# Kernel optimization log

Measured on AMD Instinct MI355X. Metric: run time of the kernel, lower is better.

The kernel has to match this reference:

```python
import jax, jax.numpy as jnp
import numpy as np

NUM_HEADS = 8

def setup_inputs() -> dict:
    key = jax.random.key(0)
    ks = jax.random.split(key, 8)
    B, T, J, N, C = 4, 16, 17, 17, 256
    x = jax.random.normal(ks[0], (B, T, J, N, C), dtype=jnp.float32)
    A_s = jax.random.uniform(ks[1], (J, J), dtype=jnp.float32)
    A_v = jax.random.uniform(ks[2], (N, N), dtype=jnp.float32)
    W_qkv = jax.random.normal(ks[3], (C, 5 * C), dtype=jnp.float32) * (C ** -0.5)
    W_proj = jax.random.normal(ks[4], (3 * C, C), dtype=jnp.float32) * ((3 * C) ** -0.5)
    b_proj = jnp.zeros((C,), dtype=jnp.float32)
    # M ~ xavier_uniform(gain=1.414) over shape (1, J, N, C)
    bound = 1.414 * np.sqrt(6.0 / (N + C))
    M = jax.random.uniform(ks[5], (1, J, N, C), dtype=jnp.float32, minval=-bound, maxval=bound)
    adj_s = jnp.full((J, J), 1e-6, dtype=jnp.float32)  # torch stores (1,1,J,J); broadcast-identical
    adj_v = jnp.full((N, N), 1e-6, dtype=jnp.float32)
    return {"x": x, "A_s": A_s, "A_v": A_v, "W_qkv": W_qkv, "W_proj": W_proj,
            "b_proj": b_proj, "M": M, "adj_s": adj_s, "adj_v": adj_v}


def reference(x, A_s, A_v, W_qkv, W_proj, b_proj, M, adj_s, adj_v):
    B, T, J, N, C = x.shape
    h = NUM_HEADS
    hc = C // h
    scale = hc ** -0.5
    bt = B * T
    xr = x.reshape(bt, J, N, C)
    # qkv Linear (no bias) then view(..., C, 5): channel-interleaved split
    qkv = (xr @ W_qkv).reshape(bt, J, N, C, 5)
    q, k, vs, vv, vsv = (qkv[..., i] * M for i in range(5))
    def heads(t):
        return t.reshape(bt, J, N, h, hc)
    q, k, vs, vv, vsv = map(heads, (q, k, vs, vv, vsv))
    # spatial attention over joints j (per node n), temporal/variate attention over n (per j)
    att_s_o = jnp.einsum('bjnhc,bknhc->bhnjk', q, k) * scale   # (bt,h,N,J,J)
    att_v_o = jnp.einsum('bjnhc,bjmhc->bhjnm', q, k) * scale   # (bt,h,J,N,N)
    att_s = jax.nn.softmax(att_s_o, axis=-1)
    att_v = jax.nn.softmax(att_v_o, axis=-1)
    # outer-product combine, algebraically separated:
    # x_vsv[b,j,n,:] = sum_{k,m} att_s[b,h,n,j,k] * att_v[b,h,j,n,m] * vsv[b,k,m,h,:]
    r = jnp.einsum('bhjnm,bkmhc->bhjnkc', att_v, vsv)           # (bt,h,J,N,J,hc)
    x_vsv = jnp.einsum('bhnjk,bhjnkc->bjnhc', att_s, r).reshape(bt, J, N, C)
    # adjacency-biased attentions (symmetrized learned bias + fixed adjacency)
    adjs = A_s + adj_s
    adjs = (adjs.T + adjs) * 0.5
    adjv = A_v + adj_v
    adjv = (adjv.T + adjv) * 0.5
    att_s2 = jax.nn.softmax(att_s_o + adjs, axis=-1)
    att_v2 = jax.nn.softmax(att_v_o + adjv, axis=-1)
    x_vs = jnp.einsum('bhnjk,bknhc->bjnhc', att_s2, vs).reshape(bt, J, N, C)
    x_vv = jnp.einsum('bhjnm,bjmhc->bjnhc', att_v2, vv).reshape(bt, J, N, C)
    out = jnp.concatenate([x_vsv, x_vs, x_vv], axis=-1) @ W_proj + b_proj
    return out.reshape(B, T, J, N, C)
```

## Files before the change

kernel.cpp:

```cpp
#include <hip/hip_runtime.h>
#include <math.h>

#define ROWS 18496
#define SCALE 0.17677669529663687f

typedef unsigned short ushort_t;
typedef __attribute__((ext_vector_type(8))) short short8;
typedef __attribute__((ext_vector_type(4))) float f32x4;

__device__ __forceinline__ void fma4(float4& d, float s, const float4& v) {
    d.x = fmaf(s, v.x, d.x); d.y = fmaf(s, v.y, d.y);
    d.z = fmaf(s, v.z, d.z); d.w = fmaf(s, v.w, d.w);
}
__device__ __forceinline__ float dot4(const float4& a, const float4& b) {
    return a.x*b.x + a.y*b.y + a.z*b.z + a.w*b.w;
}

__device__ __forceinline__ ushort_t f2bf(float x) {
    union { float f; unsigned u; } v; v.f = x;
    unsigned r = v.u + 0x7fffu + ((v.u >> 16) & 1u);
    return (ushort_t)(r >> 16);
}
__device__ __forceinline__ float bf2f(ushort_t b) {
    union { unsigned u; float f; } v; v.u = ((unsigned)b) << 16; return v.f;
}

__device__ __forceinline__ void gl_lds16(const void* g, void* l) {
    __builtin_amdgcn_global_load_lds(
        (const __attribute__((address_space(1))) void*)g,
        (__attribute__((address_space(3))) void*)l, 16, 0, 0);
}

__device__ __forceinline__ void store_hilo(ushort_t* yhi, ushort_t* ylo,
                                           size_t off, const float4& a)
{
    ushort4 h, l;
    h.x = f2bf(a.x); l.x = f2bf(a.x - bf2f(h.x));
    h.y = f2bf(a.y); l.y = f2bf(a.y - bf2f(h.y));
    h.z = f2bf(a.z); l.z = f2bf(a.z - bf2f(h.z));
    h.w = f2bf(a.w); l.w = f2bf(a.w - bf2f(h.w));
    *(ushort4*)&yhi[off] = h;
    *(ushort4*)&ylo[off] = l;
}

__global__ __launch_bounds__(256) void k_cvt_xw(
    const float4* __restrict__ x, ushort4* __restrict__ xhi, ushort4* __restrict__ xlo,
    const float* __restrict__ W, ushort_t* __restrict__ bh, ushort_t* __restrict__ bl)
{
    if (blockIdx.x < 4624) {
        int i = blockIdx.x * 256 + threadIdx.x;
        float4 v = x[i];
        ushort4 h, l;
        h.x = f2bf(v.x); l.x = f2bf(v.x - bf2f(h.x));
        h.y = f2bf(v.y); l.y = f2bf(v.y - bf2f(h.y));
        h.z = f2bf(v.z); l.z = f2bf(v.z - bf2f(h.z));
        h.w = f2bf(v.w); l.w = f2bf(v.w - bf2f(h.w));
        xhi[i] = h; xlo[i] = l;
    } else {
        int o = blockIdx.x - 4624;
        int kk = threadIdx.x;
        int col = (o & 255) * 5 + (o >> 8);
        float v = W[(size_t)kk * 1280 + col];
        ushort_t hh = f2bf(v);
        bh[(size_t)o * 256 + kk] = hh;
        bl[(size_t)o * 256 + kk] = f2bf(v - bf2f(hh));
    }
}

__global__ __launch_bounds__(256) void k_cvt_wp(
    const float* __restrict__ W, ushort_t* __restrict__ bh, ushort_t* __restrict__ bl)
{
    int n = blockIdx.x;
    for (int k = threadIdx.x; k < 768; k += 256) {
        float v = W[(size_t)k * 256 + n];
        ushort_t h = f2bf(v);
        bh[(size_t)n * 768 + k] = h;
        bl[(size_t)n * 768 + k] = f2bf(v - bf2f(h));
    }
}

template<int BM, int BN, int K, int MODE>
__global__ __launch_bounds__(256) void k_gemm(
    const ushort_t* __restrict__ Ahi, const ushort_t* __restrict__ Alo,
    const ushort_t* __restrict__ Bhi, const ushort_t* __restrict__ Blo,
    const float* __restrict__ aux,
    float* __restrict__ out)
{
    constexpr int MT = BM / 32;
    constexpr int NT = BN / 32;
    __shared__ __attribute__((aligned(16))) ushort_t sAh[BM * 32];
    __shared__ __attribute__((aligned(16))) ushort_t sAl[BM * 32];
    __shared__ __attribute__((aligned(16))) ushort_t sBh[BN * 32];
    __shared__ __attribute__((aligned(16))) ushort_t sBl[BN * 32];

    const int t = threadIdx.x;
    const int lane = t & 63;
    const int ln = lane & 15, quad = lane >> 4;
    const int wave = t >> 6;
    const int wm = wave >> 1, wn = wave & 1;
    const int m0 = blockIdx.y * BM, n0 = blockIdx.x * BN;

    f32x4 acc[MT][NT];
#pragma unroll
    for (int i = 0; i < MT; ++i)
#pragma unroll
        for (int j = 0; j < NT; ++j) acc[i][j] = (f32x4){0.f, 0.f, 0.f, 0.f};

    for (int kb = 0; kb < K; kb += 32) {
        __syncthreads();
#pragma unroll
        for (int s = t; s < BM * 4; s += 256) {
            int row = s >> 2, kc = s & 3;
            int gr = m0 + row; if (gr > ROWS - 1) gr = ROWS - 1;
            size_t gb = ((size_t)gr * K + kb) * 2 + kc * 16;
            int lb = (s & ~63) * 16;
            gl_lds16((const char*)Ahi + gb, (char*)sAh + lb);
            gl_lds16((const char*)Alo + gb, (char*)sAl + lb);
        }
#pragma unroll
        for (int s = t; s < BN * 4; s += 256) {
            int row = s >> 2, kc = s & 3;
            size_t gb = ((size_t)(n0 + row) * K + kb) * 2 + kc * 16;
            int lb = (s & ~63) * 16;
            gl_lds16((const char*)Bhi + gb, (char*)sBh + lb);
            gl_lds16((const char*)Blo + gb, (char*)sBl + lb);
        }
        __syncthreads();

        short8 ah[MT], al[MT], bh[NT], bl[NT];
#pragma unroll
        for (int i = 0; i < MT; ++i) {
            int off = (wm * (BM / 2) + i * 16 + ln) * 32 + quad * 8;
            ah[i] = *(const short8*)&sAh[off];
            al[i] = *(const short8*)&sAl[off];
        }
#pragma unroll
        for (int j = 0; j < NT; ++j) {
            int off = (wn * (BN / 2) + j * 16 + ln) * 32 + quad * 8;
            bh[j] = *(const short8*)&sBh[off];
            bl[j] = *(const short8*)&sBl[off];
        }
#pragma unroll
        for (int i = 0; i < MT; ++i)
#pragma unroll
            for (int j = 0; j < NT; ++j) {
                acc[i][j] = __builtin_amdgcn_mfma_f32_16x16x32_bf16(ah[i], bh[j], acc[i][j], 0, 0, 0);
                acc[i][j] = __builtin_amdgcn_mfma_f32_16x16x32_bf16(ah[i], bl[j], acc[i][j], 0, 0, 0);
                acc[i][j] = __builtin_amdgcn_mfma_f32_16x16x32_bf16(al[i], bh[j], acc[i][j], 0, 0, 0);
            }
    }

#pragma unroll
    for (int i = 0; i < MT; ++i) {
#pragma unroll
        for (int r = 0; r < 4; ++r) {
            int gm = m0 + wm * (BM / 2) + i * 16 + quad * 4 + r;
            if (gm >= ROWS) continue;
            if (MODE == 0) {
                int jn = gm % 289;
                const float* Mrow = &aux[(size_t)jn * 256];
#pragma unroll
                for (int j = 0; j < NT; ++j) {
                    int gn = n0 + wn * (BN / 2) + j * 16 + ln;
                    out[(size_t)gm * 1280 + gn] = acc[i][j][r] * Mrow[gn & 255];
                }
            } else {
#pragma unroll
                for (int j = 0; j < NT; ++j) {
                    int gn = n0 + wn * (BN / 2) + j * 16 + ln;
                    out[(size_t)gm * 256 + gn] = acc[i][j][r] + aux[gn];
                }
            }
        }
    }
}

__global__ __launch_bounds__(512, 2) void k_att(
    const float* __restrict__ qkv5,
    const float* __restrict__ A_s, const float* __restrict__ A_v,
    const float* __restrict__ adjS, const float* __restrict__ adjV,
    ushort_t* __restrict__ yhi, ushort_t* __restrict__ ylo)
{
    __shared__ __attribute__((aligned(16))) float sm[16184];
    float* aS  = sm;
    float* aV  = sm + 4913;
    float* ebS = sm + 9826;
    float* ebV = sm + 10115;
    float* buf = sm + 10404;

    const int t  = threadIdx.x;
    const int bh = blockIdx.x;
    const int b  = bh >> 3, h = bh & 7;
    const size_t rowbase = (size_t)b * 289;

    for (int idx = t; idx < 578; idx += 512) {
        int f = idx / 289, rem = idx % 289;
        int jj = rem / 17, kk = rem % 17;
        float bias;
        if (f == 0)
            bias = 0.5f * ((A_s[jj*17+kk] + adjS[jj*17+kk]) + (A_s[kk*17+jj] + adjS[kk*17+jj]));
        else
            bias = 0.5f * ((A_v[jj*17+kk] + adjV[jj*17+kk]) + (A_v[kk*17+jj] + adjV[kk*17+jj]));
        (f ? ebV : ebS)[rem] = expf(bias);
    }

    for (int ch = 0; ch < 2; ++ch) {
        __syncthreads();
        for (int idx = t; idx < 1156; idx += 512) {
            int p = idx >> 2, c = idx & 3;
            *(float4*)&buf[p * 20 + c * 4] =
                *(const float4*)&qkv5[(rowbase + p) * 1280 + 256 + h * 32 + ch * 16 + c * 4];
        }
        __syncthreads();
        for (int u = t; u < 578; u += 512) {
            const bool isS = (u < 289);
            const int p = isS ? u : u - 289;
            const float* qp = &qkv5[(rowbase + p) * 1280 + h * 32 + ch * 16];
            float4 q0 = *(const float4*)&qp[0];
            float4 q1 = *(const float4*)&qp[4];
            float4 q2 = *(const float4*)&qp[8];
            float4 q3 = *(const float4*)&qp[12];
            const int a = p / 17, bb = p % 17;
            float tmp[17];
            if (isS) {
#pragma unroll
                for (int kk = 0; kk < 17; ++kk) {
                    const float4* r = (const float4*)&buf[(kk * 17 + bb) * 20];
                    tmp[kk] = dot4(q0, r[0]) + dot4(q1, r[1]) + dot4(q2, r[2]) + dot4(q3, r[3]);
                }
                float* dst = &aS[bb * 289 + a * 17];
                if (ch == 0) {
#pragma unroll
                    for (int kk = 0; kk < 17; ++kk) dst[kk] = tmp[kk];
                } else {
#pragma unroll
                    for (int kk = 0; kk < 17; ++kk) dst[kk] += tmp[kk];
                }
            } else {
#pragma unroll
                for (int mm = 0; mm < 17; ++mm) {
                    const float4* r = (const float4*)&buf[(a * 17 + mm) * 20];
                    tmp[mm] = dot4(q0, r[0]) + dot4(q1, r[1]) + dot4(q2, r[2]) + dot4(q3, r[3]);
                }
                float* dst = &aV[a * 289 + bb * 17];
                if (ch == 0) {
#pragma unroll
                    for (int mm = 0; mm < 17; ++mm) dst[mm] = tmp[mm];
                } else {
#pragma unroll
                    for (int mm = 0; mm < 17; ++mm) dst[mm] += tmp[mm];
                }
            }
        }
    }
    __syncthreads();

    for (int idx = t; idx < 578; idx += 512) {
        float* row = (idx < 289) ? &aS[idx * 17] : &aV[(idx - 289) * 17];
        float v[17];
#pragma unroll
        for (int kk = 0; kk < 17; ++kk) v[kk] = row[kk] * SCALE;
        float mx = v[0];
#pragma unroll
        for (int kk = 1; kk < 17; ++kk) mx = fmaxf(mx, v[kk]);
        float sum = 0.f;
#pragma unroll
        for (int kk = 0; kk < 17; ++kk) { v[kk] = expf(v[kk] - mx); sum += v[kk]; }
        float inv = 1.f / sum;
#pragma unroll
        for (int kk = 0; kk < 17; ++kk) row[kk] = v[kk] * inv;
    }

    for (int ch = 0; ch < 2; ++ch) {
        __syncthreads();
        for (int idx = t; idx < 1156; idx += 512) {
            int p = idx >> 2, c = idx & 3;
            *(float4*)&buf[p * 20 + c * 4] =
                *(const float4*)&qkv5[(rowbase + p) * 1280 + 1024 + h * 32 + ch * 16 + c * 4];
        }
        __syncthreads();
        for (int u = t; u < 1156; u += 512) {
            const int c4 = (u & 3) * 4;
            const int p = u >> 2;
            const int jj = p / 17, nn = p % 17;
            float eV[17];
            {
                const float* s0 = &aV[jj * 289 + nn * 17];
#pragma unroll
                for (int m = 0; m < 17; ++m) eV[m] = s0[m];
            }
            float4 acc0 = {0,0,0,0};
            for (int kk = 0; kk < 17; ++kk) {
                float4 tg0 = {0,0,0,0};
#pragma unroll
                for (int m = 0; m < 17; ++m) {
                    float4 v = *(const float4*)&buf[(kk * 17 + m) * 20 + c4];
                    fma4(tg0, eV[m], v);
                }
                fma4(acc0, aS[nn * 289 + jj * 17 + kk], tg0);
            }
            store_hilo(yhi, ylo, (rowbase + p) * 768 + h * 32 + ch * 16 + c4, acc0);
        }
    }

    for (int ch = 0; ch < 2; ++ch) {
        __syncthreads();
        for (int idx = t; idx < 1156; idx += 512) {
            int p = idx >> 2, c = idx & 3;
            *(float4*)&buf[p * 20 + c * 4] =
                *(const float4*)&qkv5[(rowbase + p) * 1280 + 512 + h * 32 + ch * 16 + c * 4];
        }
        __syncthreads();
        for (int u = t; u < 1156; u += 512) {
            const int c4 = (u & 3) * 4, rest = u >> 2;
            const int n = rest % 17, j = rest / 17;
            float w[17];
            float s = 0.f;
            const float* as = &aS[n * 289 + j * 17];
            const float* eb = &ebS[j * 17];
#pragma unroll
            for (int kk = 0; kk < 17; ++kk) { w[kk] = as[kk] * eb[kk]; s += w[kk]; }
            const float inv = 1.f / s;
            float4 a0 = {0,0,0,0};
            for (int kk = 0; kk < 17; ++kk) {
                float4 v = *(const float4*)&buf[(kk * 17 + n) * 20 + c4];
                fma4(a0, w[kk], v);
            }
            a0.x *= inv; a0.y *= inv; a0.z *= inv; a0.w *= inv;
            store_hilo(yhi, ylo, (rowbase + j * 17 + n) * 768 + 256 + h * 32 + ch * 16 + c4, a0);
        }
    }

    for (int ch = 0; ch < 2; ++ch) {
        __syncthreads();
        for (int idx = t; idx < 1156; idx += 512) {
            int p = idx >> 2, c = idx & 3;
            *(float4*)&buf[p * 20 + c * 4] =
                *(const float4*)&qkv5[(rowbase + p) * 1280 + 768 + h * 32 + ch * 16 + c * 4];
        }
        __syncthreads();
        for (int u = t; u < 1156; u += 512) {
            const int c4 = (u & 3) * 4, rest = u >> 2;
            const int j = rest % 17, n = rest / 17;
            float w[17];
            float s = 0.f;
            const float* av = &aV[j * 289 + n * 17];
            const float* eb = &ebV[n * 17];
#pragma unroll
            for (int mm = 0; mm < 17; ++mm) { w[mm] = av[mm] * eb[mm]; s += w[mm]; }
            const float inv = 1.f / s;
            float4 a0 = {0,0,0,0};
            for (int mm = 0; mm < 17; ++mm) {
                float4 v = *(const float4*)&buf[(j * 17 + mm) * 20 + c4];
                fma4(a0, w[mm], v);
            }
            a0.x *= inv; a0.y *= inv; a0.z *= inv; a0.w *= inv;
            store_hilo(yhi, ylo, (rowbase + j * 17 + n) * 768 + 512 + h * 32 + ch * 16 + c4, a0);
        }
    }
}

extern "C" void kernel_launch(void* const* d_in, const int* in_sizes, int n_in,
                              void* d_out, int out_size, void* d_ws, size_t ws_size,
                              hipStream_t stream)
{
    const float* x    = (const float*)d_in[0];
    const float* A_s  = (const float*)d_in[1];
    const float* A_v  = (const float*)d_in[2];
    const float* Wqkv = (const float*)d_in[3];
    const float* Wp   = (const float*)d_in[4];
    const float* bp   = (const float*)d_in[5];
    const float* M    = (const float*)d_in[6];
    const float* adjS = (const float*)d_in[7];
    const float* adjV = (const float*)d_in[8];
    float* out = (float*)d_out;

    char* w = (char*)d_ws;
    float*    qkv5  = (float*)w;
    ushort_t* wph   = (ushort_t*)w;
    ushort_t* wpl   = (ushort_t*)(w + 393216);
    char* R = w + 134946816;
    ushort_t* xhi = (ushort_t*)R;
    ushort_t* xlo = (ushort_t*)(R + 9469952);
    ushort_t* wqh = (ushort_t*)(R + 18939904);
    ushort_t* wql = (ushort_t*)(R + 19595264);
    ushort_t* yhi = (ushort_t*)R;
    ushort_t* ylo = (ushort_t*)(R + 28422144);

    k_cvt_xw<<<dim3(5904), 256, 0, stream>>>((const float4*)x, (ushort4*)xhi, (ushort4*)xlo,
                                             Wqkv, wqh, wql);
    k_gemm<128, 128, 256, 0><<<dim3(10, 145), 256, 0, stream>>>(xhi, xlo, wqh, wql, M, qkv5);
    k_att<<<dim3(512), 512, 0, stream>>>(qkv5, A_s, A_v, adjS, adjV, yhi, ylo);
    k_cvt_wp<<<dim3(256), 256, 0, stream>>>(Wp, wph, wpl);
    k_gemm<128, 64, 768, 1><<<dim3(4, 145), 256, 0, stream>>>(yhi, ylo, wph, wpl, bp, out);
}
```

Baseline: 309.7 us.

## Compute x_vsv outer-product attention with split-bf16 MFMA instead of scalar FMAs

Replaces the scalar float4 FMA loop for the vsv outer-product attention with a matrix-core formulation. The combined weight att_s[k]*att_v[m] is built on the fly as the A operand, and vsv is staged into LDS as hi/lo bf16 pairs. Three bf16 MFMAs (hi*hi, hi*lo, lo*hi) approximate fp32 accuracy. The 289-long reduction is processed in two halves with zero padding. This cuts ALU work on the dominant contraction but adds per-element conversion overhead and a small precision loss.

Result: faster. 297.5 us (-3.9%).

```diff
diff --git a/kernel.cpp b/kernel.cpp
--- a/kernel.cpp
+++ b/kernel.cpp
@@ -271,35 +271,95 @@
         for (int kk = 0; kk < 17; ++kk) row[kk] = v[kk] * inv;
     }
 
-    for (int ch = 0; ch < 2; ++ch) {
-        __syncthreads();
-        for (int idx = t; idx < 1156; idx += 512) {
-            int p = idx >> 2, c = idx & 3;
-            *(float4*)&buf[p * 20 + c * 4] =
-                *(const float4*)&qkv5[(rowbase + p) * 1280 + 1024 + h * 32 + ch * 16 + c * 4];
-        }
-        __syncthreads();
-        for (int u = t; u < 1156; u += 512) {
-            const int c4 = (u & 3) * 4;
-            const int p = u >> 2;
-            const int jj = p / 17, nn = p % 17;
-            float eV[17];
-            {
-                const float* s0 = &aV[jj * 289 + nn * 17];
-#pragma unroll
-                for (int m = 0; m < 17; ++m) eV[m] = s0[m];
-            }
-            float4 acc0 = {0,0,0,0};
-            for (int kk = 0; kk < 17; ++kk) {
-                float4 tg0 = {0,0,0,0};
-#pragma unroll
-                for (int m = 0; m < 17; ++m) {
-                    float4 v = *(const float4*)&buf[(kk * 17 + m) * 20 + c4];
-                    fma4(tg0, eV[m], v);
-                }
-                fma4(acc0, aS[nn * 289 + jj * 17 + kk], tg0);
-            }
-            store_hilo(yhi, ylo, (rowbase + p) * 768 + h * 32 + ch * 16 + c4, acc0);
+    {
+        const int lane = t & 63;
+        const int ln = lane & 15, quad = lane >> 4;
+        const int wave = t >> 6;
+        ushort_t* vh = (ushort_t*)buf;
+        ushort_t* vl = vh + 32 * 168;
+
+        f32x4 acc[3][2];
+#pragma unroll
+        for (int r = 0; r < 3; ++r) {
+            acc[r][0] = (f32x4){0.f,0.f,0.f,0.f};
+            acc[r][1] = (f32x4){0.f,0.f,0.f,0.f};
+        }
+
+        int sbase[3], vbase[3];
+#pragma unroll
+        for (int r = 0; r < 3; ++r) {
+            int p = (wave + 8 * r) * 16 + ln; if (p > 288) p = 288;
+            int jj = (p * 61681) >> 20;
+            int nn = p - jj * 17;
+            sbase[r] = nn * 289 + jj * 17;
+            vbase[r] = jj * 289 + nn * 17;
+        }
+
+        for (int khalf = 0; khalf < 2; ++khalf) {
+            const int qbase = khalf * 160;
+            const int V = khalf ? 129 : 160;
+            __syncthreads();
+            for (int e = t; e < 5376; e += 512) {
+                if (e % 168 >= V) { vh[e] = 0; vl[e] = 0; }
+            }
+            for (int e = t; e < 32 * V; e += 512) {
+                int ql = e >> 5, c = e & 31;
+                float v = qkv5[(rowbase + qbase + ql) * 1280 + 1024 + h * 32 + c];
+                ushort_t hh = f2bf(v);
+                vh[c * 168 + ql] = hh;
+                vl[c * 168 + ql] = f2bf(v - bf2f(hh));
+            }
+            __syncthreads();
+#pragma unroll
+            for (int kstep = 0; kstep < 5; ++kstep) {
+                const int q0 = qbase + kstep * 32 + quad * 8;
+                const int lb = kstep * 32 + quad * 8;
+                short8 b0h = *(const short8*)&vh[ln * 168 + lb];
+                short8 b0l = *(const short8*)&vl[ln * 168 + lb];
+                short8 b1h = *(const short8*)&vh[(16 + ln) * 168 + lb];
+                short8 b1l = *(const short8*)&vl[(16 + ln) * 168 + lb];
+#pragma unroll
+                for (int r = 0; r < 3; ++r) {
+                    if (r == 2 && wave >= 3) continue;
+                    short8 ah, al;
+#pragma unroll
+                    for (int i = 0; i < 8; ++i) {
+                        int q = q0 + i;
+                        int qc = (q < 289) ? q : 288;
+                        int k17 = (qc * 61681) >> 20;
+                        int m17 = qc - k17 * 17;
+                        float pv = aS[sbase[r] + k17] * aV[vbase[r] + m17];
+                        pv = (q < 289) ? pv : 0.f;
+                        ushort_t ph = f2bf(pv);
+                        ah[i] = (short)ph;
+                        al[i] = (short)f2bf(pv - bf2f(ph));
+                    }
+                    acc[r][0] = __builtin_amdgcn_mfma_f32_16x16x32_bf16(ah, b0h, acc[r][0], 0, 0, 0);
+                    acc[r][0] = __builtin_amdgcn_mfma_f32_16x16x32_bf16(ah, b0l, acc[r][0], 0, 0, 0);
+                    acc[r][0] = __builtin_amdgcn_mfma_f32_16x16x32_bf16(al, b0h, acc[r][0], 0, 0, 0);
+                    acc[r][1] = __builtin_amdgcn_mfma_f32_16x16x32_bf16(ah, b1h, acc[r][1], 0, 0, 0);
+                    acc[r][1] = __builtin_amdgcn_mfma_f32_16x16x32_bf16(ah, b1l, acc[r][1], 0, 0, 0);
+                    acc[r][1] = __builtin_amdgcn_mfma_f32_16x16x32_bf16(al, b1h, acc[r][1], 0, 0, 0);
+                }
+            }
+        }
+#pragma unroll
+        for (int r = 0; r < 3; ++r) {
+            int rt = wave + 8 * r;
+            if (rt >= 19) continue;
+#pragma unroll
+            for (int ct = 0; ct < 2; ++ct) {
+#pragma unroll
+                for (int rr = 0; rr < 4; ++rr) {
+                    int p = rt * 16 + quad * 4 + rr;
+                    if (p > 288) continue;
+                    float v = acc[r][ct][rr];
+                    ushort_t hh = f2bf(v);
+                    size_t off = (rowbase + p) * 768 + h * 32 + ct * 16 + ln;
+                    yhi[off] = hh;
+                    ylo[off] = f2bf(v - bf2f(hh));
+                }
+            }
         }
     }
 
```
